# Kernel optimization log

Measured on AMD Instinct MI355X. Metric: run time of the kernel, lower is better.

## Reference

```python
import jax, jax.numpy as jnp
import numpy as np

D_MODEL = 1024
N_HEADS = 16
D_H = D_MODEL // N_HEADS
MAX_LEN = 2048
BATCH = 2
SEQ = 2048
EPS = 1e-8
W_SCALE = 0.02


def _rms_norm(x, w):
    # RMSNorm: x * rsqrt(mean(x^2) + eps) * w
    ms = jnp.mean(jnp.square(x), axis=-1, keepdims=True)
    return w * (x * jax.lax.rsqrt(ms + EPS))


def setup_inputs() -> dict:
    key = jax.random.key(0)
    ks = jax.random.split(key, 12)
    d = D_MODEL
    inp = {
        "x": jax.random.normal(ks[0], (BATCH, SEQ, d), dtype=jnp.float32),
        "t_bias": jnp.zeros((1,), dtype=jnp.float32),  # unused by the module
        "p_bias": jax.random.normal(ks[1], (MAX_LEN, N_HEADS), dtype=jnp.float32),
        # AMS layer params (Linear stored as [in, out])
        "wq": jax.random.normal(ks[2], (d, d), dtype=jnp.float32) * W_SCALE,
        "bq": jnp.zeros((d,), dtype=jnp.float32),
        "wk": jax.random.normal(ks[3], (d, d), dtype=jnp.float32) * W_SCALE,
        "bk": jnp.zeros((d,), dtype=jnp.float32),
        "wv": jax.random.normal(ks[4], (d, d), dtype=jnp.float32) * W_SCALE,
        "bv": jnp.zeros((d,), dtype=jnp.float32),
        "wu": jax.random.normal(ks[5], (d, d), dtype=jnp.float32) * W_SCALE,
        "bu": jnp.zeros((d,), dtype=jnp.float32),
        "g_ams": jnp.ones((d,), dtype=jnp.float32),   # shared RMSNorm weight in AMSLayer
        # MFFN layer params
        "w0": jax.random.normal(ks[6], (d, d), dtype=jnp.float32) * W_SCALE,
        "b0": jnp.zeros((d,), dtype=jnp.float32),
        "w1": jax.random.normal(ks[7], (d, 2 * d), dtype=jnp.float32) * W_SCALE,
        "b1": jnp.zeros((2 * d,), dtype=jnp.float32),
        "w2": jax.random.normal(ks[8], (d, d), dtype=jnp.float32) * W_SCALE,
        "b2": jnp.zeros((d,), dtype=jnp.float32),
        "g_mffn": jnp.ones((d,), dtype=jnp.float32),
    }
    return inp


def reference(x, t_bias, p_bias, wq, bq, wk, bk, wv, bv, wu, bu, g_ams,
              w0, b0, w1, b1, w2, b2, g_mffn):
    B, S, d = x.shape
    H, dh = N_HEADS, D_H

    # ---- AMS layer ----
    x_norm = _rms_norm(x, g_ams)

    def proj(w, b):
        # [B,S,d] -> [B,H,S,dh]
        return (x_norm @ w + b).reshape(B, S, H, dh).transpose(0, 2, 1, 3)

    q = proj(wq, bq)
    k = proj(wk, bk)
    v = proj(wv, bv)

    scale = 1.0 / np.sqrt(dh).astype(np.float32)
    score = jnp.einsum('bhsd,bhtd->bhst', q, k) * scale
    # additive positional bias: p_bias[:S].T -> [H,S], broadcast over query dim
    score = score + p_bias[:S, :].T[None, :, None, :]

    attn = jax.nn.silu(score)                        # SiLU instead of softmax
    out = jnp.einsum('bhst,bhtd->bhsd', attn, v)
    out = out.transpose(0, 2, 1, 3).reshape(B, S, d)

    u = jax.nn.silu(x_norm @ wu + bu)
    ams_out = _rms_norm(out, g_ams) * u

    # ---- MFFN layer ----
    o = (ams_out @ w0 + b0) + x
    o_norm = _rms_norm(o, g_mffn)
    x12 = o_norm @ w1 + b1
    x1, x2 = jnp.split(x12, 2, axis=-1)
    swiglu = jax.nn.silu(x1) * x2
    return (swiglu @ w2 + b2) + o
```

## Files before the change

### kernel.cpp

```cpp
#include <hip/hip_runtime.h>
#include <stdint.h>
#include <math.h>


#define D    1024
#define NH   16
#define DH   64
#define B_   2
#define S_   2048
#define ROWS 4096
#define LQ   4096
#define EPSR 1e-8f

typedef unsigned short u16;
typedef __attribute__((ext_vector_type(8))) short short8;
typedef __attribute__((ext_vector_type(4))) float f32x4;
typedef __attribute__((ext_vector_type(16))) float f32x16;
typedef __attribute__((ext_vector_type(4))) int int4v;

__device__ __forceinline__ float bf2f(u16 u) {
    union { uint32_t i; float f; } c; c.i = ((uint32_t)u) << 16; return c.f;
}
__device__ __forceinline__ u16 f2bf(float f) {
    union { float f; uint32_t i; } c; c.f = f;
    uint32_t x = c.i;
    x += 0x7fffu + ((x >> 16) & 1u);
    return (u16)(x >> 16);
}
#define LOG2E 1.44269504f
__device__ __forceinline__ float silu_fast(float v) {
    return v * __builtin_amdgcn_rcpf(1.0f + __builtin_amdgcn_exp2f(v * -LOG2E));
}

__global__ __launch_bounds__(256) void transpose_all_kernel(
    const float* __restrict__ wq, const float* __restrict__ wk,
    const float* __restrict__ wv, const float* __restrict__ wu,
    const float* __restrict__ w0, const float* __restrict__ w2,
    const float* __restrict__ w1,
    u16* __restrict__ wT4, u16* __restrict__ w0T,
    u16* __restrict__ w2T, u16* __restrict__ w1T)
{
    const unsigned MI = 1u << 20;
    const int z = blockIdx.z;
    const float* W; u16* WT; int N; int noff = 0;
    switch (z) {
        case 0: W = wq; WT = wT4;          N = 1024; break;
        case 1: W = wk; WT = wT4 + 1 * MI; N = 1024; break;
        case 2: W = wv; WT = wT4 + 2 * MI; N = 1024; break;
        case 3: W = wu; WT = wT4 + 3 * MI; N = 1024; break;
        case 4: W = w0; WT = w0T;          N = 1024; break;
        case 5: W = w2; WT = w2T;          N = 1024; break;
        case 6: W = w1; WT = w1T;          N = 2048; noff = 0;    break;
        default:W = w1; WT = w1T;          N = 2048; noff = 1024; break;
    }
    __shared__ float T[64][65];
    const int tid = threadIdx.x;
    const int n0 = (blockIdx.x << 6) + noff;
    const int k0 = blockIdx.y << 6;
    const int rr = tid >> 4;
    const int cc = (tid & 15) << 2;
#pragma unroll
    for (int l = 0; l < 4; ++l) {
        const int r = rr + (l << 4);
        float4 v = *(const float4*)&W[(size_t)(k0 + r) * N + n0 + cc];
        T[cc + 0][r] = v.x; T[cc + 1][r] = v.y;
        T[cc + 2][r] = v.z; T[cc + 3][r] = v.w;
    }
    __syncthreads();
    const int n  = tid >> 2;
    const int ks = (tid & 3) << 4;
#pragma unroll
    for (int m = 0; m < 4; ++m) {
        const int k = ks + (m << 2);
        float4 v = *(const float4*)&T[n][k];
        ushort4 o;
        o.x = f2bf(v.x); o.y = f2bf(v.y); o.z = f2bf(v.z); o.w = f2bf(v.w);
        *(ushort4*)&WT[(size_t)(n0 + n) * 1024 + k0 + k] = o;
    }
}

__global__ __launch_bounds__(256) void pbt_kernel(
    const float* __restrict__ pb, float* __restrict__ pbT)
{
    const int tid = threadIdx.x;
    const int r = (blockIdx.x << 7) + (tid >> 1);
    const int c0 = (tid & 1) << 3;
    float4 v0 = *(const float4*)&pb[(size_t)r * NH + c0];
    float4 v1 = *(const float4*)&pb[(size_t)r * NH + c0 + 4];
    pbT[(size_t)(c0 + 0) * S_ + r] = v0.x;
    pbT[(size_t)(c0 + 1) * S_ + r] = v0.y;
    pbT[(size_t)(c0 + 2) * S_ + r] = v0.z;
    pbT[(size_t)(c0 + 3) * S_ + r] = v0.w;
    pbT[(size_t)(c0 + 4) * S_ + r] = v1.x;
    pbT[(size_t)(c0 + 5) * S_ + r] = v1.y;
    pbT[(size_t)(c0 + 6) * S_ + r] = v1.z;
    pbT[(size_t)(c0 + 7) * S_ + r] = v1.w;
}

__global__ __launch_bounds__(256) void rmsnorm_kernel(
    const float* __restrict__ inf, const u16* __restrict__ inb, int ldi,
    const float* __restrict__ g,
    const u16* __restrict__ mul, int ldm,
    u16* __restrict__ out, int ldo)
{
    const int row = blockIdx.x;
    const int tid = threadIdx.x;
    const int c = tid << 2;
    float x0, x1, x2, x3;
    if (inb) {
        ushort4 xi = *(const ushort4*)&inb[(size_t)row * ldi + c];
        x0 = bf2f(xi.x); x1 = bf2f(xi.y); x2 = bf2f(xi.z); x3 = bf2f(xi.w);
    } else {
        float4 xi = *(const float4*)&inf[(size_t)row * ldi + c];
        x0 = xi.x; x1 = xi.y; x2 = xi.z; x3 = xi.w;
    }
    float ss = x0*x0 + x1*x1 + x2*x2 + x3*x3;
#pragma unroll
    for (int off = 32; off > 0; off >>= 1) ss += __shfl_down(ss, off, 64);
    __shared__ float red[4];
    if ((tid & 63) == 0) red[tid >> 6] = ss;
    __syncthreads();
    float r = rsqrtf((red[0] + red[1] + red[2] + red[3]) * (1.0f / D) + EPSR);
    float4 gv = *(const float4*)&g[c];
    float v0 = x0 * r * gv.x, v1 = x1 * r * gv.y, v2 = x2 * r * gv.z, v3 = x3 * r * gv.w;
    if (mul) {
        ushort4 mi = *(const ushort4*)&mul[(size_t)row * ldm + c];
        v0 *= bf2f(mi.x); v1 *= bf2f(mi.y); v2 *= bf2f(mi.z); v3 *= bf2f(mi.w);
    }
    ushort4 o;
    o.x = f2bf(v0); o.y = f2bf(v1); o.z = f2bf(v2); o.w = f2bf(v3);
    *(ushort4*)&out[(size_t)row * ldo + c] = o;
}

__global__ __launch_bounds__(256) void gemm128(
    const u16* __restrict__ A, const u16* __restrict__ WT,
    const float* __restrict__ bs0, const float* __restrict__ bs1,
    const float* __restrict__ bs2, const float* __restrict__ bs3,
    u16* __restrict__ outb, int ldo, int actmask,
    u16* __restrict__ VT, int vtsel)
{
    __shared__ u16 As[128 * 32];
    __shared__ u16 Bs[128 * 32];
    const int tid  = threadIdx.x;
    const int wave = tid >> 6;
    const int lane = tid & 63;
    const int lm   = lane & 15;
    const int quad = lane >> 4;
    const int row0 = blockIdx.y << 7;
    const int col0 = blockIdx.x << 7;
    const int wr = (wave >> 1) << 6;
    const int wc = (wave & 1) << 6;

    const int srow = wave * 32 + (lane >> 2);
    const int skp  = (lane & 3) << 3;
    const u16* Ag = A  + (size_t)(row0 + srow) * 1024 + skp;
    const u16* Bg = WT + (size_t)(col0 + srow) * 1024 + skp;
    u16* Asd0 = &As[(wave * 32) * 32];
    u16* Asd1 = &As[(wave * 32 + 16) * 32];
    u16* Bsd0 = &Bs[(wave * 32) * 32];
    u16* Bsd1 = &Bs[(wave * 32 + 16) * 32];

    f32x4 acc[4][4] = {};

    for (int k0 = 0; k0 < 1024; k0 += 32) {
        __syncthreads();
        __builtin_amdgcn_global_load_lds(
            (const __attribute__((address_space(1))) void*)(Ag + k0),
            (__attribute__((address_space(3))) void*)Asd0, 16, 0, 0);
        __builtin_amdgcn_global_load_lds(
            (const __attribute__((address_space(1))) void*)(Ag + 16 * 1024 + k0),
            (__attribute__((address_space(3))) void*)Asd1, 16, 0, 0);
        __builtin_amdgcn_global_load_lds(
            (const __attribute__((address_space(1))) void*)(Bg + k0),
            (__attribute__((address_space(3))) void*)Bsd0, 16, 0, 0);
        __builtin_amdgcn_global_load_lds(
            (const __attribute__((address_space(1))) void*)(Bg + 16 * 1024 + k0),
            (__attribute__((address_space(3))) void*)Bsd1, 16, 0, 0);
        __syncthreads();
        short8 af[4], bf[4];
#pragma unroll
        for (int i = 0; i < 4; ++i)
            af[i] = *(const short8*)&As[(wr + i * 16 + lm) * 32 + quad * 8];
#pragma unroll
        for (int j = 0; j < 4; ++j)
            bf[j] = *(const short8*)&Bs[(wc + j * 16 + lm) * 32 + quad * 8];
#pragma unroll
        for (int i = 0; i < 4; ++i)
#pragma unroll
            for (int j = 0; j < 4; ++j)
                acc[i][j] = __builtin_amdgcn_mfma_f32_16x16x32_bf16(af[i], bf[j], acc[i][j], 0, 0, 0);
    }
    const int sel = col0 >> 10;
    const float* bias = (sel == 0) ? bs0 : (sel == 1) ? bs1 : (sel == 2) ? bs2 : bs3;
    const int act = (actmask >> sel) & 1;
    if (VT && sel == vtsel) {
        const int b = row0 >> 11;
#pragma unroll
        for (int j = 0; j < 4; ++j) {
            const int c2 = (col0 + wc + j * 16 + lm) & 1023;
            const int h  = c2 >> 6;
            const int dh = c2 & 63;
            const float bj = bias[c2];
            u16* vrow = VT + ((size_t)(b * NH + h) * 64 + dh) * (size_t)S_;
#pragma unroll
            for (int i = 0; i < 4; ++i) {
                const int tb = (row0 & 2047) + wr + i * 16 + quad * 4;
                ushort4 o;
                o.x = f2bf(acc[i][j][0] + bj);
                o.y = f2bf(acc[i][j][1] + bj);
                o.z = f2bf(acc[i][j][2] + bj);
                o.w = f2bf(acc[i][j][3] + bj);
                *(ushort4*)&vrow[tb] = o;
            }
        }
    } else {
#pragma unroll
        for (int j = 0; j < 4; ++j) {
            const int colg = col0 + wc + j * 16 + lm;
            const float bj = bias[colg & 1023];
#pragma unroll
            for (int i = 0; i < 4; ++i) {
#pragma unroll
                for (int r = 0; r < 4; ++r) {
                    const int rowg = row0 + wr + i * 16 + quad * 4 + r;
                    float v = acc[i][j][r] + bj;
                    if (act) v = silu_fast(v);
                    outb[(size_t)rowg * ldo + colg] = f2bf(v);
                }
            }
        }
    }
}

__global__ __launch_bounds__(256) void gemm64(
    const u16* __restrict__ A, int lda, const u16* __restrict__ WT,
    const float* __restrict__ bias,
    const float* __restrict__ res,
    float* __restrict__ outf, int ldo)
{
    __shared__ u16 As[128 * 32];
    __shared__ u16 Bs[64 * 32];
    const int tid  = threadIdx.x;
    const int wave = tid >> 6;
    const int lane = tid & 63;
    const int lm   = lane & 15;
    const int quad = lane >> 4;
    const int row0 = blockIdx.y << 7;
    const int col0 = blockIdx.x << 6;
    const int wr = (wave >> 1) << 6;
    const int wc = (wave & 1) << 5;

    const int srA = wave * 32 + (lane >> 2);
    const int srB = wave * 16 + (lane >> 2);
    const int skp = (lane & 3) << 3;
    const u16* Ag = A  + (size_t)(row0 + srA) * lda + skp;
    const u16* Bg = WT + (size_t)(col0 + srB) * 1024 + skp;
    u16* Asd0 = &As[(wave * 32) * 32];
    u16* Asd1 = &As[(wave * 32 + 16) * 32];
    u16* Bsd  = &Bs[(wave * 16) * 32];

    f32x4 acc[4][2] = {};

    for (int k0 = 0; k0 < 1024; k0 += 32) {
        __syncthreads();
        __builtin_amdgcn_global_load_lds(
            (const __attribute__((address_space(1))) void*)(Ag + k0),
            (__attribute__((address_space(3))) void*)Asd0, 16, 0, 0);
        __builtin_amdgcn_global_load_lds(
            (const __attribute__((address_space(1))) void*)(Ag + (size_t)16 * lda + k0),
            (__attribute__((address_space(3))) void*)Asd1, 16, 0, 0);
        __builtin_amdgcn_global_load_lds(
            (const __attribute__((address_space(1))) void*)(Bg + k0),
            (__attribute__((address_space(3))) void*)Bsd, 16, 0, 0);
        __syncthreads();
        short8 af[4], bf[2];
#pragma unroll
        for (int i = 0; i < 4; ++i)
            af[i] = *(const short8*)&As[(wr + i * 16 + lm) * 32 + quad * 8];
#pragma unroll
        for (int j = 0; j < 2; ++j)
            bf[j] = *(const short8*)&Bs[(wc + j * 16 + lm) * 32 + quad * 8];
#pragma unroll
        for (int i = 0; i < 4; ++i)
#pragma unroll
            for (int j = 0; j < 2; ++j)
                acc[i][j] = __builtin_amdgcn_mfma_f32_16x16x32_bf16(af[i], bf[j], acc[i][j], 0, 0, 0);
    }
#pragma unroll
    for (int j = 0; j < 2; ++j) {
        const int colg = col0 + wc + j * 16 + lm;
        const float bj = bias[colg];
#pragma unroll
        for (int i = 0; i < 4; ++i) {
#pragma unroll
            for (int r = 0; r < 4; ++r) {
                const int rowg = row0 + wr + i * 16 + quad * 4 + r;
                const size_t idx = (size_t)rowg * ldo + colg;
                float v = acc[i][j][r] + bj;
                if (res) v += res[idx];
                outf[idx] = v;
            }
        }
    }
}

__global__ __launch_bounds__(256) void gemm_w1_swiglu(
    const u16* __restrict__ A, const u16* __restrict__ WT,
    const float* __restrict__ b1, u16* __restrict__ outb)
{
    __shared__ u16 As[128 * 32];
    __shared__ u16 Bs[128 * 32];
    const int tid  = threadIdx.x;
    const int wave = tid >> 6;
    const int lane = tid & 63;
    const int lm   = lane & 15;
    const int quad = lane >> 4;
    const int row0 = blockIdx.y << 7;
    const int col0 = blockIdx.x << 6;
    const int wr  = (wave >> 1) << 6;
    const int wc2 = (wave & 1) << 5;

    const int srow = wave * 32 + (lane >> 2);
    const int skp  = (lane & 3) << 3;
    const int brow = col0 + (srow & 63) + ((srow >> 6) << 10);
    const u16* Ag = A  + (size_t)(row0 + srow) * 1024 + skp;
    const u16* Bg = WT + (size_t)brow * 1024 + skp;
    u16* Asd0 = &As[(wave * 32) * 32];
    u16* Asd1 = &As[(wave * 32 + 16) * 32];
    u16* Bsd0 = &Bs[(wave * 32) * 32];
    u16* Bsd1 = &Bs[(wave * 32 + 16) * 32];

    f32x4 acc[4][4] = {};

    for (int k0 = 0; k0 < 1024; k0 += 32) {
        __syncthreads();
        __builtin_amdgcn_global_load_lds(
            (const __attribute__((address_space(1))) void*)(Ag + k0),
            (__attribute__((address_space(3))) void*)Asd0, 16, 0, 0);
        __builtin_amdgcn_global_load_lds(
            (const __attribute__((address_space(1))) void*)(Ag + 16 * 1024 + k0),
            (__attribute__((address_space(3))) void*)Asd1, 16, 0, 0);
        __builtin_amdgcn_global_load_lds(
            (const __attribute__((address_space(1))) void*)(Bg + k0),
            (__attribute__((address_space(3))) void*)Bsd0, 16, 0, 0);
        __builtin_amdgcn_global_load_lds(
            (const __attribute__((address_space(1))) void*)(Bg + 16 * 1024 + k0),
            (__attribute__((address_space(3))) void*)Bsd1, 16, 0, 0);
        __syncthreads();
        short8 af[4], bf[4];
#pragma unroll
        for (int i = 0; i < 4; ++i)
            af[i] = *(const short8*)&As[(wr + i * 16 + lm) * 32 + quad * 8];
#pragma unroll
        for (int j = 0; j < 2; ++j) {
            bf[j]     = *(const short8*)&Bs[(wc2 + j * 16 + lm) * 32 + quad * 8];
            bf[j + 2] = *(const short8*)&Bs[(64 + wc2 + j * 16 + lm) * 32 + quad * 8];
        }
#pragma unroll
        for (int i = 0; i < 4; ++i)
#pragma unroll
            for (int j = 0; j < 4; ++j)
                acc[i][j] = __builtin_amdgcn_mfma_f32_16x16x32_bf16(af[i], bf[j], acc[i][j], 0, 0, 0);
    }
#pragma unroll
    for (int j = 0; j < 2; ++j) {
        const int colg = col0 + wc2 + j * 16 + lm;
        const float ba = b1[colg];
        const float bb = b1[1024 + colg];
#pragma unroll
        for (int i = 0; i < 4; ++i) {
#pragma unroll
            for (int r = 0; r < 4; ++r) {
                const int rowg = row0 + wr + i * 16 + quad * 4 + r;
                const float x1v = acc[i][j][r] + ba;
                const float x2v = acc[i][j + 2][r] + bb;
                outb[(size_t)rowg * LQ + colg] = f2bf(silu_fast(x1v) * x2v);
            }
        }
    }
}

__global__ __launch_bounds__(512, 2) void attn_mfma(
    const u16* __restrict__ qkvu, const u16* __restrict__ VT,
    const float* __restrict__ pbT, u16* __restrict__ out)
{
    __shared__ u16 Ks[2][2][64 * 64];
    __shared__ u16 Vs[2][2][64 * 64];
    __shared__ float pbl[S_];
    const int tid  = threadIdx.x;
    const int wave = tid >> 6;
    const int grp  = wave >> 2;
    const int wq4  = wave & 3;
    const int lane = tid & 63;
    const int l31  = lane & 31;
    const int hi   = lane >> 5;
    const int l7   = lane & 7;
    const int xorv = l7 ^ ((l31 >> 3) & 3);
    const int flat = blockIdx.x + (blockIdx.y << 4) + (blockIdx.z << 8);
    const int work = ((flat & 7) << 6) + (flat >> 3);
    const int s0 = (work & 15) << 7;
    const int h  = (work >> 4) & 15;
    const int b  = work >> 8;
    const size_t base = (size_t)b * S_ * LQ + (size_t)h * DH;
    const u16* q  = qkvu + base;
    const u16* kg = qkvu + base + 1024;
    const u16* vt = VT + (size_t)(b * NH + h) * 64 * S_;
    const float* pbh = pbT + (size_t)h * S_;

    for (int i = tid * 4; i < S_; i += 2048)
        *(float4*)&pbl[i] = *(const float4*)&pbh[i];

    const int qrow = s0 + wq4 * 32 + l31;
    short8 qf[4];
#pragma unroll
    for (int i = 0; i < 4; ++i)
        qf[i] = *(const short8*)&q[(size_t)qrow * LQ + i * 16 + hi * 8];

    const int lr  = lane >> 3;
    const int gA  = (2 * wq4) & 3;
    const int gB  = (2 * wq4 + 1) & 3;
    const u16* kgA = kg + (size_t)(16 * wq4 + lr) * LQ     + ((l7 ^ lr ^ gA) << 3);
    const u16* kgB = kg + (size_t)(16 * wq4 + 8 + lr) * LQ + ((l7 ^ lr ^ gB) << 3);
    const u16* vgA = vt + (size_t)(16 * wq4 + lr) * S_     + ((l7 ^ lr ^ gA) << 3);
    const u16* vgB = vt + (size_t)(16 * wq4 + 8 + lr) * S_ + ((l7 ^ lr ^ gB) << 3);

#define GLDS(gp, lp) __builtin_amdgcn_global_load_lds( \
        (const __attribute__((address_space(1))) void*)(gp), \
        (__attribute__((address_space(3))) void*)(lp), 16, 0, 0)
#define ISSUE(it, bu) do { \
        const size_t tn = ((size_t)(grp) * 16 + (size_t)(it)) << 6; \
        GLDS(kgA + tn * LQ, &Ks[grp][bu][(16 * wq4) * 64]); \
        GLDS(kgB + tn * LQ, &Ks[grp][bu][(16 * wq4 + 8) * 64]); \
        GLDS(vgA + tn,      &Vs[grp][bu][(16 * wq4) * 64]); \
        GLDS(vgB + tn,      &Vs[grp][bu][(16 * wq4 + 8) * 64]); \
    } while (0)

    f32x16 accO[2] = {};
    ISSUE(0, 0);
    __syncthreads();

#pragma unroll 1
    for (int it = 0; it < 16; ++it) {
        const int ib = it & 1;
        const int nb = ib ^ 1;
        if (it + 1 < 16) ISSUE(it + 1, nb);
        const int t0 = grp * 1024 + (it << 6);
        f32x16 st0 = {}, st1 = {};
        __builtin_amdgcn_s_setprio(1);
#pragma unroll
        for (int i = 0; i < 4; ++i) {
            const int co = ((2 * i + hi) ^ xorv) << 3;
            short8 kf0 = *(const short8*)&Ks[grp][ib][(l31) * 64 + co];
            short8 kf1 = *(const short8*)&Ks[grp][ib][(32 + l31) * 64 + co];
            st0 = __builtin_amdgcn_mfma_f32_32x32x16_bf16(kf0, qf[i], st0, 0, 0, 0);
            st1 = __builtin_amdgcn_mfma_f32_32x32x16_bf16(kf1, qf[i], st1, 0, 0, 0);
        }
        __builtin_amdgcn_s_setprio(0);
        int pk0[8], pk1[8];
#pragma unroll
        for (int g = 0; g < 4; ++g) {
            float4 pbv0 = *(const float4*)&pbl[t0 + 8 * g + 4 * hi];
            float4 pbv1 = *(const float4*)&pbl[t0 + 32 + 8 * g + 4 * hi];
            float a0 = silu_fast(fmaf(st0[4 * g + 0], 0.125f, pbv0.x));
            float a1 = silu_fast(fmaf(st0[4 * g + 1], 0.125f, pbv0.y));
            float a2 = silu_fast(fmaf(st0[4 * g + 2], 0.125f, pbv0.z));
            float a3 = silu_fast(fmaf(st0[4 * g + 3], 0.125f, pbv0.w));
            float b0 = silu_fast(fmaf(st1[4 * g + 0], 0.125f, pbv1.x));
            float b1 = silu_fast(fmaf(st1[4 * g + 1], 0.125f, pbv1.y));
            float b2 = silu_fast(fmaf(st1[4 * g + 2], 0.125f, pbv1.z));
            float b3 = silu_fast(fmaf(st1[4 * g + 3], 0.125f, pbv1.w));
            asm("v_cvt_pk_bf16_f32 %0, %1, %2" : "=v"(pk0[2 * g])     : "v"(a0), "v"(a1));
            asm("v_cvt_pk_bf16_f32 %0, %1, %2" : "=v"(pk0[2 * g + 1]) : "v"(a2), "v"(a3));
            asm("v_cvt_pk_bf16_f32 %0, %1, %2" : "=v"(pk1[2 * g])     : "v"(b0), "v"(b1));
            asm("v_cvt_pk_bf16_f32 %0, %1, %2" : "=v"(pk1[2 * g + 1]) : "v"(b2), "v"(b3));
        }
#pragma unroll
        for (int m = 0; m < 2; ++m) {
            int w0 = pk0[4 * m + 0], w2 = pk0[4 * m + 2];
            int w1 = pk0[4 * m + 1], w3 = pk0[4 * m + 3];
            asm("v_permlane32_swap_b32 %0, %1" : "+v"(w0), "+v"(w2));
            asm("v_permlane32_swap_b32 %0, %1" : "+v"(w1), "+v"(w3));
            int u0 = pk1[4 * m + 0], u2 = pk1[4 * m + 2];
            int u1 = pk1[4 * m + 1], u3 = pk1[4 * m + 3];
            asm("v_permlane32_swap_b32 %0, %1" : "+v"(u0), "+v"(u2));
            asm("v_permlane32_swap_b32 %0, %1" : "+v"(u1), "+v"(u3));
            union { int4v i; short8 s; } pa, pb2;
            pa.i.x  = w0; pa.i.y  = w1; pa.i.z  = w2; pa.i.w  = w3;
            pb2.i.x = u0; pb2.i.y = u1; pb2.i.z = u2; pb2.i.w = u3;
            __builtin_amdgcn_s_setprio(1);
#pragma unroll
            for (int n = 0; n < 2; ++n) {
                short8 vf0 = *(const short8*)&Vs[grp][ib][(32 * n + l31) * 64 +
                    (((2 * m + hi) ^ xorv) << 3)];
                short8 vf1 = *(const short8*)&Vs[grp][ib][(32 * n + l31) * 64 +
                    (((4 + 2 * m + hi) ^ xorv) << 3)];
                accO[n] = __builtin_amdgcn_mfma_f32_32x32x16_bf16(pa.s,  vf0, accO[n], 0, 0, 0);
                accO[n] = __builtin_amdgcn_mfma_f32_32x32x16_bf16(pb2.s, vf1, accO[n], 0, 0, 0);
            }
            __builtin_amdgcn_s_setprio(0);
        }
        __syncthreads();
    }
#undef ISSUE
#undef GLDS
    float* scr = (float*)&Ks[0][0][0];
    const int sl = wq4 * 64 + lane;
    if (grp == 1) {
#pragma unroll
        for (int n = 0; n < 2; ++n)
#pragma unroll
            for (int r = 0; r < 16; ++r)
                scr[(n * 16 + r) * 256 + sl] = accO[n][r];
    }
    __syncthreads();
    if (grp == 0) {
#pragma unroll
        for (int n = 0; n < 2; ++n)
#pragma unroll
            for (int r = 0; r < 16; ++r)
                accO[n][r] += scr[(n * 16 + r) * 256 + sl];
        const int qb = s0 + wq4 * 32 + 4 * hi;
#pragma unroll
        for (int n = 0; n < 2; ++n)
#pragma unroll
            for (int r = 0; r < 16; ++r) {
                const int qq = qb + (r & 3) + 8 * (r >> 2);
                out[base + (size_t)qq * LQ + 32 * n + l31] = f2bf(accO[n][r]);
            }
    }
}

extern "C" void kernel_launch(void* const* d_in, const int* in_sizes, int n_in,
                              void* d_out, int out_size, void* d_ws, size_t ws_size,
                              hipStream_t stream)
{
    const float* x      = (const float*)d_in[0];
    const float* pb     = (const float*)d_in[2];
    const float* wq     = (const float*)d_in[3];
    const float* bq     = (const float*)d_in[4];
    const float* wk     = (const float*)d_in[5];
    const float* bk     = (const float*)d_in[6];
    const float* wv     = (const float*)d_in[7];
    const float* bv     = (const float*)d_in[8];
    const float* wu     = (const float*)d_in[9];
    const float* bu     = (const float*)d_in[10];
    const float* g_ams  = (const float*)d_in[11];
    const float* w0     = (const float*)d_in[12];
    const float* b0     = (const float*)d_in[13];
    const float* w1     = (const float*)d_in[14];
    const float* b1     = (const float*)d_in[15];
    const float* w2     = (const float*)d_in[16];
    const float* b2     = (const float*)d_in[17];
    const float* g_mffn = (const float*)d_in[18];
    float* OUT = (float*)d_out;
    u16*   VT  = (u16*)d_out;
    float* pbT = (float*)((u16*)d_out + 4 * (1u << 20));

    const size_t MI = 1024 * 1024;
    u16* WS   = (u16*)d_ws;
    u16* wT4  = WS;
    u16* w0T  = WS + 4 * MI;
    u16* w2T  = WS + 5 * MI;
    u16* w1T  = WS + 6 * MI;
    u16* A0   = WS + 8 * MI;
    u16* QKVU = WS + 12 * MI;

    dim3 blk(256);

    transpose_all_kernel<<<dim3(16, 16, 8), blk, 0, stream>>>(
        wq, wk, wv, wu, w0, w2, w1, wT4, w0T, w2T, w1T);
    pbt_kernel<<<16, blk, 0, stream>>>(pb, pbT);

    rmsnorm_kernel<<<ROWS, blk, 0, stream>>>(x, nullptr, D, g_ams, nullptr, 0, A0, D);
    gemm128<<<dim3(32, 32), blk, 0, stream>>>(A0, wT4, bq, bk, bv, bu,
                                              QKVU, LQ, 0b1000, VT, 2);
    attn_mfma<<<dim3(16, 16, 2), dim3(512), 0, stream>>>(QKVU, VT, pbT, QKVU);
    rmsnorm_kernel<<<ROWS, blk, 0, stream>>>(nullptr, QKVU, LQ, g_ams, QKVU + 3072, LQ, A0, D);
    gemm64<<<dim3(16, 32), blk, 0, stream>>>(A0, D, w0T, b0, x, OUT, D);
    rmsnorm_kernel<<<ROWS, blk, 0, stream>>>(OUT, nullptr, D, g_mffn, nullptr, 0, A0, D);
    gemm_w1_swiglu<<<dim3(16, 32), blk, 0, stream>>>(A0, w1T, b1, QKVU + 2048);
    gemm64<<<dim3(16, 32), blk, 0, stream>>>(QKVU + 2048, LQ, w2T, b2, OUT, OUT, D);
    (void)ws_size; (void)in_sizes; (void)n_in; (void)out_size;
}
```

Before: 322.2 us.

## Deepen GEMM K-tile to 64 with XOR-swizzled LDS, XCD remap, merge pbT transpose

All three GEMM kernels now stage a 64-wide K slice per iteration instead of 32. This halves the number of barrier pairs, and the LDS layout uses an XOR swizzle on the global-to-LDS copies to avoid bank conflicts on the fragment reads. Workgroup IDs are remapped so that consecutive tiles land on the same XCD, which should improve L2 reuse. The positional-bias transpose is folded into the weight transpose launch as an extra z-slice, removing one kernel launch. LDS use per block doubles, which may reduce occupancy.

```diff
diff --git a/kernel.cpp b/kernel.cpp
--- a/kernel.cpp
+++ b/kernel.cpp
@@ -32,16 +32,42 @@
     return v * __builtin_amdgcn_rcpf(1.0f + __builtin_amdgcn_exp2f(v * -LOG2E));
 }
 
+#define GLDS16(gp, lp) __builtin_amdgcn_global_load_lds( \
+        (const __attribute__((address_space(1))) void*)(gp), \
+        (__attribute__((address_space(3))) void*)(lp), 16, 0, 0)
+
+__device__ __forceinline__ int xcd_work(int flat, int nwg) {
+    return ((flat & 7) * (nwg >> 3)) + (flat >> 3);
+}
+
 __global__ __launch_bounds__(256) void transpose_all_kernel(
     const float* __restrict__ wq, const float* __restrict__ wk,
     const float* __restrict__ wv, const float* __restrict__ wu,
     const float* __restrict__ w0, const float* __restrict__ w2,
     const float* __restrict__ w1,
     u16* __restrict__ wT4, u16* __restrict__ w0T,
-    u16* __restrict__ w2T, u16* __restrict__ w1T)
+    u16* __restrict__ w2T, u16* __restrict__ w1T,
+    const float* __restrict__ pb, float* __restrict__ pbT)
 {
     const unsigned MI = 1u << 20;
     const int z = blockIdx.z;
+    const int tid = threadIdx.x;
+    if (z == 8) {
+        if (blockIdx.y != 0) return;
+        const int r = (blockIdx.x << 7) + (tid >> 1);
+        const int c0 = (tid & 1) << 3;
+        float4 v0 = *(const float4*)&pb[(size_t)r * NH + c0];
+        float4 v1 = *(const float4*)&pb[(size_t)r * NH + c0 + 4];
+        pbT[(size_t)(c0 + 0) * S_ + r] = v0.x;
+        pbT[(size_t)(c0 + 1) * S_ + r] = v0.y;
+        pbT[(size_t)(c0 + 2) * S_ + r] = v0.z;
+        pbT[(size_t)(c0 + 3) * S_ + r] = v0.w;
+        pbT[(size_t)(c0 + 4) * S_ + r] = v1.x;
+        pbT[(size_t)(c0 + 5) * S_ + r] = v1.y;
+        pbT[(size_t)(c0 + 6) * S_ + r] = v1.z;
+        pbT[(size_t)(c0 + 7) * S_ + r] = v1.w;
+        return;
+    }
     const float* W; u16* WT; int N; int noff = 0;
     switch (z) {
         case 0: W = wq; WT = wT4;          N = 1024; break;
@@ -54,7 +80,6 @@
         default:W = w1; WT = w1T;          N = 2048; noff = 1024; break;
     }
     __shared__ float T[64][65];
-    const int tid = threadIdx.x;
     const int n0 = (blockIdx.x << 6) + noff;
     const int k0 = blockIdx.y << 6;
     const int rr = tid >> 4;
@@ -77,24 +102,6 @@
         o.x = f2bf(v.x); o.y = f2bf(v.y); o.z = f2bf(v.z); o.w = f2bf(v.w);
         *(ushort4*)&WT[(size_t)(n0 + n) * 1024 + k0 + k] = o;
     }
-}
-
-__global__ __launch_bounds__(256) void pbt_kernel(
-    const float* __restrict__ pb, float* __restrict__ pbT)
-{
-    const int tid = threadIdx.x;
-    const int r = (blockIdx.x << 7) + (tid >> 1);
-    const int c0 = (tid & 1) << 3;
-    float4 v0 = *(const float4*)&pb[(size_t)r * NH + c0];
-    float4 v1 = *(const float4*)&pb[(size_t)r * NH + c0 + 4];
-    pbT[(size_t)(c0 + 0) * S_ + r] = v0.x;
-    pbT[(size_t)(c0 + 1) * S_ + r] = v0.y;
-    pbT[(size_t)(c0 + 2) * S_ + r] = v0.z;
-    pbT[(size_t)(c0 + 3) * S_ + r] = v0.w;
-    pbT[(size_t)(c0 + 4) * S_ + r] = v1.x;
-    pbT[(size_t)(c0 + 5) * S_ + r] = v1.y;
-    pbT[(size_t)(c0 + 6) * S_ + r] = v1.z;
-    pbT[(size_t)(c0 + 7) * S_ + r] = v1.w;
 }
 
 __global__ __launch_bounds__(256) void rmsnorm_kernel(
@@ -139,56 +146,55 @@
     u16* __restrict__ outb, int ldo, int actmask,
     u16* __restrict__ VT, int vtsel)
 {
-    __shared__ u16 As[128 * 32];
-    __shared__ u16 Bs[128 * 32];
+    __shared__ u16 As[128 * 64];
+    __shared__ u16 Bs[128 * 64];
     const int tid  = threadIdx.x;
     const int wave = tid >> 6;
     const int lane = tid & 63;
     const int lm   = lane & 15;
     const int quad = lane >> 4;
-    const int row0 = blockIdx.y << 7;
-    const int col0 = blockIdx.x << 7;
+    const int l7   = lm & 7;
+    const int gx   = gridDim.x;
+    const int gxm  = gx - 1;
+    const int gxs  = __popc(gxm);
+    const int work = xcd_work(blockIdx.x + (blockIdx.y << gxs), gx * gridDim.y);
+    const int col0 = (work & gxm) << 7;
+    const int row0 = (work >> gxs) << 7;
     const int wr = (wave >> 1) << 6;
     const int wc = (wave & 1) << 6;
 
-    const int srow = wave * 32 + (lane >> 2);
-    const int skp  = (lane & 3) << 3;
-    const u16* Ag = A  + (size_t)(row0 + srow) * 1024 + skp;
-    const u16* Bg = WT + (size_t)(col0 + srow) * 1024 + skp;
-    u16* Asd0 = &As[(wave * 32) * 32];
-    u16* Asd1 = &As[(wave * 32 + 16) * 32];
-    u16* Bsd0 = &Bs[(wave * 32) * 32];
-    u16* Bsd1 = &Bs[(wave * 32 + 16) * 32];
+    const int lr8  = lane >> 3;
+    const int gch8 = ((lane & 7) ^ lr8) << 3;
+    const u16* Ag = A  + (size_t)(row0 + wave * 32 + lr8) * 1024 + gch8;
+    const u16* Bg = WT + (size_t)(col0 + wave * 32 + lr8) * 1024 + gch8;
 
     f32x4 acc[4][4] = {};
 
-    for (int k0 = 0; k0 < 1024; k0 += 32) {
-        __syncthreads();
-        __builtin_amdgcn_global_load_lds(
-            (const __attribute__((address_space(1))) void*)(Ag + k0),
-            (__attribute__((address_space(3))) void*)Asd0, 16, 0, 0);
-        __builtin_amdgcn_global_load_lds(
-            (const __attribute__((address_space(1))) void*)(Ag + 16 * 1024 + k0),
-            (__attribute__((address_space(3))) void*)Asd1, 16, 0, 0);
-        __builtin_amdgcn_global_load_lds(
-            (const __attribute__((address_space(1))) void*)(Bg + k0),
-            (__attribute__((address_space(3))) void*)Bsd0, 16, 0, 0);
-        __builtin_amdgcn_global_load_lds(
-            (const __attribute__((address_space(1))) void*)(Bg + 16 * 1024 + k0),
-            (__attribute__((address_space(3))) void*)Bsd1, 16, 0, 0);
-        __syncthreads();
-        short8 af[4], bf[4];
-#pragma unroll
-        for (int i = 0; i < 4; ++i)
-            af[i] = *(const short8*)&As[(wr + i * 16 + lm) * 32 + quad * 8];
-#pragma unroll
-        for (int j = 0; j < 4; ++j)
-            bf[j] = *(const short8*)&Bs[(wc + j * 16 + lm) * 32 + quad * 8];
-#pragma unroll
-        for (int i = 0; i < 4; ++i)
+    for (int k0 = 0; k0 < 1024; k0 += 64) {
+        __syncthreads();
+#pragma unroll
+        for (int j = 0; j < 4; ++j) {
+            GLDS16(Ag + (size_t)(8 * j) * 1024 + k0, &As[(wave * 32 + 8 * j) * 64]);
+            GLDS16(Bg + (size_t)(8 * j) * 1024 + k0, &Bs[(wave * 32 + 8 * j) * 64]);
+        }
+        __syncthreads();
+#pragma unroll
+        for (int kk = 0; kk < 2; ++kk) {
+            short8 af[4], bf[4];
+#pragma unroll
+            for (int i = 0; i < 4; ++i)
+                af[i] = *(const short8*)&As[(wr + i * 16 + lm) * 64 +
+                                            (((kk * 4 + quad) ^ l7) << 3)];
 #pragma unroll
             for (int j = 0; j < 4; ++j)
-                acc[i][j] = __builtin_amdgcn_mfma_f32_16x16x32_bf16(af[i], bf[j], acc[i][j], 0, 0, 0);
+                bf[j] = *(const short8*)&Bs[(wc + j * 16 + lm) * 64 +
+                                            (((kk * 4 + quad) ^ l7) << 3)];
+#pragma unroll
+            for (int i = 0; i < 4; ++i)
+#pragma unroll
+                for (int j = 0; j < 4; ++j)
+                    acc[i][j] = __builtin_amdgcn_mfma_f32_16x16x32_bf16(af[i], bf[j], acc[i][j], 0, 0, 0);
+        }
     }
     const int sel = col0 >> 10;
     const float* bias = (sel == 0) ? bs0 : (sel == 1) ? bs1 : (sel == 2) ? bs2 : bs3;
@@ -238,53 +244,56 @@
     const float* __restrict__ res,
     float* __restrict__ outf, int ldo)
 {
-    __shared__ u16 As[128 * 32];
-    __shared__ u16 Bs[64 * 32];
+    __shared__ u16 As[128 * 64];
+    __shared__ u16 Bs[64 * 64];
     const int tid  = threadIdx.x;
     const int wave = tid >> 6;
     const int lane = tid & 63;
     const int lm   = lane & 15;
     const int quad = lane >> 4;
-    const int row0 = blockIdx.y << 7;
-    const int col0 = blockIdx.x << 6;
+    const int l7   = lm & 7;
+    const int gx   = gridDim.x;
+    const int gxm  = gx - 1;
+    const int gxs  = __popc(gxm);
+    const int work = xcd_work(blockIdx.x + (blockIdx.y << gxs), gx * gridDim.y);
+    const int col0 = (work & gxm) << 6;
+    const int row0 = (work >> gxs) << 7;
     const int wr = (wave >> 1) << 6;
     const int wc = (wave & 1) << 5;
 
-    const int srA = wave * 32 + (lane >> 2);
-    const int srB = wave * 16 + (lane >> 2);
-    const int skp = (lane & 3) << 3;
-    const u16* Ag = A  + (size_t)(row0 + srA) * lda + skp;
-    const u16* Bg = WT + (size_t)(col0 + srB) * 1024 + skp;
-    u16* Asd0 = &As[(wave * 32) * 32];
-    u16* Asd1 = &As[(wave * 32 + 16) * 32];
-    u16* Bsd  = &Bs[(wave * 16) * 32];
+    const int lr8  = lane >> 3;
+    const int gch8 = ((lane & 7) ^ lr8) << 3;
+    const u16* Ag = A  + (size_t)(row0 + wave * 32 + lr8) * lda + gch8;
+    const u16* Bg = WT + (size_t)(col0 + wave * 16 + lr8) * 1024 + gch8;
 
     f32x4 acc[4][2] = {};
 
-    for (int k0 = 0; k0 < 1024; k0 += 32) {
-        __syncthreads();
-        __builtin_amdgcn_global_load_lds(
-            (const __attribute__((address_space(1))) void*)(Ag + k0),
-            (__attribute__((address_space(3))) void*)Asd0, 16, 0, 0);
-        __builtin_amdgcn_global_load_lds(
-            (const __attribute__((address_space(1))) void*)(Ag + (size_t)16 * lda + k0),
-            (__attribute__((address_space(3))) void*)Asd1, 16, 0, 0);
-        __builtin_amdgcn_global_load_lds(
-            (const __attribute__((address_space(1))) void*)(Bg + k0),
-            (__attribute__((address_space(3))) void*)Bsd, 16, 0, 0);
-        __syncthreads();
-        short8 af[4], bf[2];
-#pragma unroll
-        for (int i = 0; i < 4; ++i)
-            af[i] = *(const short8*)&As[(wr + i * 16 + lm) * 32 + quad * 8];
+    for (int k0 = 0; k0 < 1024; k0 += 64) {
+        __syncthreads();
+#pragma unroll
+        for (int j = 0; j < 4; ++j)
+            GLDS16(Ag + (size_t)(8 * j) * lda + k0, &As[(wave * 32 + 8 * j) * 64]);
 #pragma unroll
         for (int j = 0; j < 2; ++j)
-            bf[j] = *(const short8*)&Bs[(wc + j * 16 + lm) * 32 + quad * 8];
-#pragma unroll
-        for (int i = 0; i < 4; ++i)
+            GLDS16(Bg + (size_t)(8 * j) * 1024 + k0, &Bs[(wave * 16 + 8 * j) * 64]);
+        __syncthreads();
+#pragma unroll
+        for (int kk = 0; kk < 2; ++kk) {
+            short8 af[4], bf[2];
+#pragma unroll
+            for (int i = 0; i < 4; ++i)
+                af[i] = *(const short8*)&As[(wr + i * 16 + lm) * 64 +
+                                            (((kk * 4 + quad) ^ l7) << 3)];
 #pragma unroll
             for (int j = 0; j < 2; ++j)
-                acc[i][j] = __builtin_amdgcn_mfma_f32_16x16x32_bf16(af[i], bf[j], acc[i][j], 0, 0, 0);
+                bf[j] = *(const short8*)&Bs[(wc + j * 16 + lm) * 64 +
+                                            (((kk * 4 + quad) ^ l7) << 3)];
+#pragma unroll
+            for (int i = 0; i < 4; ++i)
+#pragma unroll
+                for (int j = 0; j < 2; ++j)
+                    acc[i][j] = __builtin_amdgcn_mfma_f32_16x16x32_bf16(af[i], bf[j], acc[i][j], 0, 0, 0);
+        }
     }
 #pragma unroll
     for (int j = 0; j < 2; ++j) {
@@ -308,59 +317,60 @@
     const u16* __restrict__ A, const u16* __restrict__ WT,
     const float* __restrict__ b1, u16* __restrict__ outb)
 {
-    __shared__ u16 As[128 * 32];
-    __shared__ u16 Bs[128 * 32];
+    __shared__ u16 As[128 * 64];
+    __shared__ u16 Bs[128 * 64];
     const int tid  = threadIdx.x;
     const int wave = tid >> 6;
     const int lane = tid & 63;
     const int lm   = lane & 15;
     const int quad = lane >> 4;
-    const int row0 = blockIdx.y << 7;
-    const int col0 = blockIdx.x << 6;
+    const int l7   = lm & 7;
+    const int gx   = gridDim.x;
+    const int gxm  = gx - 1;
+    const int gxs  = __popc(gxm);
+    const int work = xcd_work(blockIdx.x + (blockIdx.y << gxs), gx * gridDim.y);
+    const int col0 = (work & gxm) << 6;
+    const int row0 = (work >> gxs) << 7;
     const int wr  = (wave >> 1) << 6;
     const int wc2 = (wave & 1) << 5;
 
-    const int srow = wave * 32 + (lane >> 2);
-    const int skp  = (lane & 3) << 3;
-    const int brow = col0 + (srow & 63) + ((srow >> 6) << 10);
-    const u16* Ag = A  + (size_t)(row0 + srow) * 1024 + skp;
-    const u16* Bg = WT + (size_t)brow * 1024 + skp;
-    u16* Asd0 = &As[(wave * 32) * 32];
-    u16* Asd1 = &As[(wave * 32 + 16) * 32];
-    u16* Bsd0 = &Bs[(wave * 32) * 32];
-    u16* Bsd1 = &Bs[(wave * 32 + 16) * 32];
+    const int lr8  = lane >> 3;
+    const int gch8 = ((lane & 7) ^ lr8) << 3;
+    const int sb   = wave * 32;
+    const int brow = col0 + (sb & 63) + ((sb >> 6) << 10) + lr8;
+    const u16* Ag = A  + (size_t)(row0 + wave * 32 + lr8) * 1024 + gch8;
+    const u16* Bg = WT + (size_t)brow * 1024 + gch8;
 
     f32x4 acc[4][4] = {};
 
-    for (int k0 = 0; k0 < 1024; k0 += 32) {
-        __syncthreads();
-        __builtin_amdgcn_global_load_lds(
-            (const __attribute__((address_space(1))) void*)(Ag + k0),
-            (__attribute__((address_space(3))) void*)Asd0, 16, 0, 0);
-        __builtin_amdgcn_global_load_lds(
-            (const __attribute__((address_space(1))) void*)(Ag + 16 * 1024 + k0),
-            (__attribute__((address_space(3))) void*)Asd1, 16, 0, 0);
-        __builtin_amdgcn_global_load_lds(
-            (const __attribute__((address_space(1))) void*)(Bg + k0),
-            (__attribute__((address_space(3))) void*)Bsd0, 16, 0, 0);
-        __builtin_amdgcn_global_load_lds(
-            (const __attribute__((address_space(1))) void*)(Bg + 16 * 1024 + k0),
-            (__attribute__((address_space(3))) void*)Bsd1, 16, 0, 0);
-        __syncthreads();
-        short8 af[4], bf[4];
-#pragma unroll
-        for (int i = 0; i < 4; ++i)
-            af[i] = *(const short8*)&As[(wr + i * 16 + lm) * 32 + quad * 8];
-#pragma unroll
-        for (int j = 0; j < 2; ++j) {
-            bf[j]     = *(const short8*)&Bs[(wc2 + j * 16 + lm) * 32 + quad * 8];
-            bf[j + 2] = *(const short8*)&Bs[(64 + wc2 + j * 16 + lm) * 32 + quad * 8];
-        }
-#pragma unroll
-        for (int i = 0; i < 4; ++i)
-#pragma unroll
-            for (int j = 0; j < 4; ++j)
-                acc[i][j] = __builtin_amdgcn_mfma_f32_16x16x32_bf16(af[i], bf[j], acc[i][j], 0, 0, 0);
+    for (int k0 = 0; k0 < 1024; k0 += 64) {
+        __syncthreads();
+#pragma unroll
+        for (int j = 0; j < 4; ++j) {
+            GLDS16(Ag + (size_t)(8 * j) * 1024 + k0, &As[(wave * 32 + 8 * j) * 64]);
+            GLDS16(Bg + (size_t)(8 * j) * 1024 + k0, &Bs[(wave * 32 + 8 * j) * 64]);
+        }
+        __syncthreads();
+#pragma unroll
+        for (int kk = 0; kk < 2; ++kk) {
+            short8 af[4], bf[4];
+#pragma unroll
+            for (int i = 0; i < 4; ++i)
+                af[i] = *(const short8*)&As[(wr + i * 16 + lm) * 64 +
+                                            (((kk * 4 + quad) ^ l7) << 3)];
+#pragma unroll
+            for (int j = 0; j < 2; ++j) {
+                bf[j]     = *(const short8*)&Bs[(wc2 + j * 16 + lm) * 64 +
+                                                (((kk * 4 + quad) ^ l7) << 3)];
+                bf[j + 2] = *(const short8*)&Bs[(64 + wc2 + j * 16 + lm) * 64 +
+                                                (((kk * 4 + quad) ^ l7) << 3)];
+            }
+#pragma unroll
+            for (int i = 0; i < 4; ++i)
+#pragma unroll
+                for (int j = 0; j < 4; ++j)
+                    acc[i][j] = __builtin_amdgcn_mfma_f32_16x16x32_bf16(af[i], bf[j], acc[i][j], 0, 0, 0);
+        }
     }
 #pragma unroll
     for (int j = 0; j < 2; ++j) {
@@ -424,15 +434,12 @@
     const u16* vgA = vt + (size_t)(16 * wq4 + lr) * S_     + ((l7 ^ lr ^ gA) << 3);
     const u16* vgB = vt + (size_t)(16 * wq4 + 8 + lr) * S_ + ((l7 ^ lr ^ gB) << 3);
 
-#define GLDS(gp, lp) __builtin_amdgcn_global_load_lds( \
-        (const __attribute__((address_space(1))) void*)(gp), \
-        (__attribute__((address_space(3))) void*)(lp), 16, 0, 0)
 #define ISSUE(it, bu) do { \
         const size_t tn = ((size_t)(grp) * 16 + (size_t)(it)) << 6; \
-        GLDS(kgA + tn * LQ, &Ks[grp][bu][(16 * wq4) * 64]); \
-        GLDS(kgB + tn * LQ, &Ks[grp][bu][(16 * wq4 + 8) * 64]); \
-        GLDS(vgA + tn,      &Vs[grp][bu][(16 * wq4) * 64]); \
-        GLDS(vgB + tn,      &Vs[grp][bu][(16 * wq4 + 8) * 64]); \
+        GLDS16(kgA + tn * LQ, &Ks[grp][bu][(16 * wq4) * 64]); \
+        GLDS16(kgB + tn * LQ, &Ks[grp][bu][(16 * wq4 + 8) * 64]); \
+        GLDS16(vgA + tn,      &Vs[grp][bu][(16 * wq4) * 64]); \
+        GLDS16(vgB + tn,      &Vs[grp][bu][(16 * wq4 + 8) * 64]); \
     } while (0)
 
     f32x16 accO[2] = {};
@@ -502,7 +509,6 @@
         __syncthreads();
     }
 #undef ISSUE
-#undef GLDS
     float* scr = (float*)&Ks[0][0][0];
     const int sl = wq4 * 64 + lane;
     if (grp == 1) {
@@ -567,9 +573,8 @@
 
     dim3 blk(256);
 
-    transpose_all_kernel<<<dim3(16, 16, 8), blk, 0, stream>>>(
-        wq, wk, wv, wu, w0, w2, w1, wT4, w0T, w2T, w1T);
-    pbt_kernel<<<16, blk, 0, stream>>>(pb, pbT);
+    transpose_all_kernel<<<dim3(16, 16, 9), blk, 0, stream>>>(
+        wq, wk, wv, wu, w0, w2, w1, wT4, w0T, w2T, w1T, pb, pbT);
 
     rmsnorm_kernel<<<ROWS, blk, 0, stream>>>(x, nullptr, D, g_ams, nullptr, 0, A0, D);
     gemm128<<<dim3(32, 32), blk, 0, stream>>>(A0, wT4, bq, bk, bv, bu,
```

Result: faster. 297.8 us (-7.6%).
